# Optimization experiments

Hardware: AMD Instinct MI355X
Metric: run time of the kernel (lower is better)

## Reference

```python
import jax, jax.numpy as jnp
import numpy as np

# Module config (matches init_kwargs)
SHAPE = (32, 32)          # wire grid
KERNEL = (3, 3)           # window per dim
NUM_LAYERS = 4
NINPUTS = int(np.prod(KERNEL))        # 9
NPOS = 2 ** NINPUTS                   # 512 possible boolean input combos


def _bitmask():
    # itertools.product(range(2), repeat=NINPUTS) then transpose -> (NINPUTS, NPOS)
    # combination j, window-element m has bit (j >> (NINPUTS-1-m)) & 1
    j = jnp.arange(NPOS)
    m = jnp.arange(NINPUTS)
    return ((j[None, :] >> (NINPUTS - 1 - m)[:, None]) & 1).astype(jnp.float32)


def _convolve(x):
    # x: (B, H, W) -> (B, H, W, K) wrapped sliding windows (im2col via rolls),
    # faithful to ASIC.convolve with kernel_offset='center'.
    out = x
    for d, k in enumerate(KERNEL):
        # window element i along dim d comes from position +i (wraparound)
        out = jnp.stack([jnp.roll(out, -i, axis=1 + d) for i in range(k)], axis=out.ndim)
    out = out.reshape(x.shape + (-1,))  # (B, H, W, K) with k0 slowest-varying
    # 'center' offset: roll by prod((k-1)//2) along the LAST spatial dim (as the torch code does)
    shift = int(np.prod([(k - 1) // 2 for k in KERNEL]))
    out = jnp.roll(out, shift, axis=len(KERNEL))  # axis = last spatial axis in (B, H, W, K)
    return out


def setup_inputs() -> dict:
    key = jax.random.key(0)
    k1, k2 = jax.random.split(key)
    x = jax.random.uniform(k1, (16,) + SHAPE, dtype=jnp.float32)
    toggle_gates = jax.random.uniform(k2, (NUM_LAYERS, NPOS) + SHAPE, dtype=jnp.float32)
    return {"x": x, "toggle_gates": toggle_gates}


def reference(x, toggle_gates):
    tw = jax.nn.sigmoid(toggle_gates)       # (L, NPOS, H, W)
    bits = _bitmask()                        # (NINPUTS, NPOS)
    # embed(): shape == x spatial shape -> stride-1 slices; initial state is x, output is full state
    state = x                                # (B, H, W)
    for layer in range(NUM_LAYERS):
        conv = _convolve(state)              # (B, H, W, K)
        # soft-LUT weights: prod over window elems of (1 - |bit - input|)
        w = jnp.prod(1.0 - jnp.abs(conv[..., None] - bits), axis=-2)  # (B, H, W, NPOS)
        state = jnp.clip(jnp.einsum('bhwp,phw->bhw', w, tw[layer]), 0.0, 1.0)
    return state
```

## Files before the change

### kernel.cpp

```cpp
#include <hip/hip_runtime.h>

#define HH 32
#define WW 32
#define NB 16
#define NPOS 512
#define TILE 8
#define PPAD 516
#define NTHR 512

__global__ __launch_bounds__(NTHR) void asic_layer(
    const float* __restrict__ src,
    const float* __restrict__ tg,
    float* __restrict__ dst)
{
    __shared__ float lut[TILE * PPAD];
    __shared__ float red[NTHR];

    const int t   = threadIdx.x;
    const int hw0 = blockIdx.x * TILE;

    #pragma unroll
    for (int k = 0; k < 8; ++k) {
        int f   = t + NTHR * k;
        int p   = f >> 3;
        int pos = f & 7;
        float g = tg[p * (HH * WW) + hw0 + pos];
        lut[pos * PPAD + p] = 1.0f / (1.0f + __expf(-g));
    }

    const int c   = t & 127;
    const int q   = t >> 7;
    const int b   = c >> 3;
    const int hwl = c & 7;
    const int h   = hw0 >> 5;
    const int w   = (hw0 & 31) + hwl;

    float cc[9];
    const float* sb = src + b * (HH * WW);
    #pragma unroll
    for (int i = 0; i < 3; ++i) {
        int row = ((h + i) & 31) * 32;
        #pragma unroll
        for (int j = 0; j < 3; ++j) {
            cc[3 * i + j] = sb[row + ((w + j - 1 + 32) & 31)];
        }
    }

    __syncthreads();

    float v[32];
    {
        float a2[2], a4[4], a8[8], a16[16];
        a2[0] = 1.0f - cc[4]; a2[1] = cc[4];
        #pragma unroll
        for (int i = 0; i < 2; ++i)  { a4[2*i]  = a2[i]  * (1.0f - cc[5]); a4[2*i+1]  = a2[i]  * cc[5]; }
        #pragma unroll
        for (int i = 0; i < 4; ++i)  { a8[2*i]  = a4[i]  * (1.0f - cc[6]); a8[2*i+1]  = a4[i]  * cc[6]; }
        #pragma unroll
        for (int i = 0; i < 8; ++i)  { a16[2*i] = a8[i]  * (1.0f - cc[7]); a16[2*i+1] = a8[i]  * cc[7]; }
        #pragma unroll
        for (int i = 0; i < 16; ++i) { v[2*i]   = a16[i] * (1.0f - cc[8]); v[2*i+1]   = a16[i] * cc[8]; }
    }
    float u[16];
    {
        float a2[2], a4[4], a8[8];
        a2[0] = 1.0f - cc[0]; a2[1] = cc[0];
        #pragma unroll
        for (int i = 0; i < 2; ++i) { a4[2*i] = a2[i] * (1.0f - cc[1]); a4[2*i+1] = a2[i] * cc[1]; }
        #pragma unroll
        for (int i = 0; i < 4; ++i) { a8[2*i] = a4[i] * (1.0f - cc[2]); a8[2*i+1] = a4[i] * cc[2]; }
        #pragma unroll
        for (int i = 0; i < 8; ++i) { u[2*i]  = a8[i] * (1.0f - cc[3]); u[2*i+1]  = a8[i] * cc[3]; }
    }

    const float4* lut4 = (const float4*)(lut + hwl * PPAD);
    float acc = 0.0f;
    #pragma unroll
    for (int hh = 0; hh < 4; ++hh) {
        int hi = 4 * q + hh;
        float ps0 = 0.f, ps1 = 0.f, ps2 = 0.f, ps3 = 0.f;
        #pragma unroll
        for (int l4 = 0; l4 < 8; ++l4) {
            float4 L = lut4[hi * 8 + l4];
            ps0 = fmaf(L.x, v[4*l4+0], ps0);
            ps1 = fmaf(L.y, v[4*l4+1], ps1);
            ps2 = fmaf(L.z, v[4*l4+2], ps2);
            ps3 = fmaf(L.w, v[4*l4+3], ps3);
        }
        acc = fmaf(u[hi], (ps0 + ps1) + (ps2 + ps3), acc);
    }

    red[t] = acc;
    __syncthreads();

    if (t < 128) {
        float s = (red[t] + red[t + 128]) + (red[t + 256] + red[t + 384]);
        s = fminf(fmaxf(s, 0.0f), 1.0f);
        dst[b * (HH * WW) + h * 32 + w] = s;
    }
}

extern "C" void kernel_launch(void* const* d_in, const int* in_sizes, int n_in,
                              void* d_out, int out_size, void* d_ws, size_t ws_size,
                              hipStream_t stream) {
    const float* x  = (const float*)d_in[0];
    const float* tg = (const float*)d_in[1];
    float* out = (float*)d_out;
    float* ws  = (float*)d_ws;

    const int grid = (HH * WW) / TILE;
    const size_t L = (size_t)NPOS * HH * WW;

    asic_layer<<<grid, NTHR, 0, stream>>>(x,   tg + 0 * L, ws);
    asic_layer<<<grid, NTHR, 0, stream>>>(ws,  tg + 1 * L, out);
    asic_layer<<<grid, NTHR, 0, stream>>>(out, tg + 2 * L, ws);
    asic_layer<<<grid, NTHR, 0, stream>>>(ws,  tg + 3 * L, out);
}
```

Baseline: 78.30 us.

## Fuse four layer launches into one persistent kernel with grid barriers

Merges the four per-layer kernel launches into a single persistent kernel of 128 blocks. Each block prefetches and sigmoids the LUT slices for all four layers into shared memory up front, and a global atomic counter barrier separates the layers. This removes three launch gaps and lets the toggle-gate loads for later layers overlap with earlier work. In exchange it uses four times the LDS per block, adds a memset, and depends on all 128 blocks being co-resident for the spin barrier to be safe.

```diff
diff --git a/kernel.cpp b/kernel.cpp
--- a/kernel.cpp
+++ b/kernel.cpp
@@ -7,26 +7,33 @@
 #define TILE 8
 #define PPAD 516
 #define NTHR 512
+#define NBLK 128
+#define NLAYERS 4
 
-__global__ __launch_bounds__(NTHR) void asic_layer(
-    const float* __restrict__ src,
+__device__ __forceinline__ void grid_barrier(int* cnt) {
+    __syncthreads();
+    if (threadIdx.x == 0) {
+        __hip_atomic_fetch_add(cnt, 1, __ATOMIC_RELEASE, __HIP_MEMORY_SCOPE_AGENT);
+        while (__hip_atomic_load(cnt, __ATOMIC_ACQUIRE, __HIP_MEMORY_SCOPE_AGENT) < NBLK) {
+            __builtin_amdgcn_s_sleep(16);
+        }
+    }
+    __syncthreads();
+}
+
+__global__ __launch_bounds__(NTHR) void asic_fused(
+    const float* __restrict__ x,
     const float* __restrict__ tg,
-    float* __restrict__ dst)
+    float* __restrict__ bufA,
+    float* __restrict__ bufB,
+    float* __restrict__ out,
+    int* __restrict__ bar)
 {
-    __shared__ float lut[TILE * PPAD];
+    __shared__ float lut[NLAYERS][TILE * PPAD];
     __shared__ float red[NTHR];
 
     const int t   = threadIdx.x;
     const int hw0 = blockIdx.x * TILE;
-
-    #pragma unroll
-    for (int k = 0; k < 8; ++k) {
-        int f   = t + NTHR * k;
-        int p   = f >> 3;
-        int pos = f & 7;
-        float g = tg[p * (HH * WW) + hw0 + pos];
-        lut[pos * PPAD + p] = 1.0f / (1.0f + __expf(-g));
-    }
 
     const int c   = t & 127;
     const int q   = t >> 7;
@@ -35,68 +42,89 @@
     const int h   = hw0 >> 5;
     const int w   = (hw0 & 31) + hwl;
 
-    float cc[9];
-    const float* sb = src + b * (HH * WW);
     #pragma unroll
-    for (int i = 0; i < 3; ++i) {
-        int row = ((h + i) & 31) * 32;
-        #pragma unroll
-        for (int j = 0; j < 3; ++j) {
-            cc[3 * i + j] = sb[row + ((w + j - 1 + 32) & 31)];
-        }
+    for (int k = 0; k < 32; ++k) {
+        int f     = t + NTHR * k;
+        int layer = f >> 12;
+        int r     = f & 4095;
+        int p     = r >> 3;
+        int pos   = r & 7;
+        float g = tg[(size_t)layer * NPOS * HH * WW + p * (HH * WW) + hw0 + pos];
+        lut[layer][pos * PPAD + p] = 1.0f / (1.0f + __expf(-g));
     }
 
-    __syncthreads();
+    const float* src = x;
 
-    float v[32];
-    {
-        float a2[2], a4[4], a8[8], a16[16];
-        a2[0] = 1.0f - cc[4]; a2[1] = cc[4];
+    for (int layer = 0; layer < NLAYERS; ++layer) {
+        float* dst = (layer == 3) ? out : ((layer & 1) ? bufB : bufA);
+
+        float cc[9];
+        const float* sb = src + b * (HH * WW);
         #pragma unroll
-        for (int i = 0; i < 2; ++i)  { a4[2*i]  = a2[i]  * (1.0f - cc[5]); a4[2*i+1]  = a2[i]  * cc[5]; }
+        for (int i = 0; i < 3; ++i) {
+            int row = ((h + i) & 31) * 32;
+            #pragma unroll
+            for (int j = 0; j < 3; ++j) {
+                cc[3 * i + j] = sb[row + ((w + j - 1 + 32) & 31)];
+            }
+        }
+
+        if (layer == 0) __syncthreads();
+
+        float v[32];
+        {
+            float a2[2], a4[4], a8[8], a16[16];
+            a2[0] = 1.0f - cc[4]; a2[1] = cc[4];
+            #pragma unroll
+            for (int i = 0; i < 2; ++i)  { a4[2*i]  = a2[i]  * (1.0f - cc[5]); a4[2*i+1]  = a2[i]  * cc[5]; }
+            #pragma unroll
+            for (int i = 0; i < 4; ++i)  { a8[2*i]  = a4[i]  * (1.0f - cc[6]); a8[2*i+1]  = a4[i]  * cc[6]; }
+            #pragma unroll
+            for (int i = 0; i < 8; ++i)  { a16[2*i] = a8[i]  * (1.0f - cc[7]); a16[2*i+1] = a8[i]  * cc[7]; }
+            #pragma unroll
+            for (int i = 0; i < 16; ++i) { v[2*i]   = a16[i] * (1.0f - cc[8]); v[2*i+1]   = a16[i] * cc[8]; }
+        }
+        float u[16];
+        {
+            float a2[2], a4[4], a8[8];
+            a2[0] = 1.0f - cc[0]; a2[1] = cc[0];
+            #pragma unroll
+            for (int i = 0; i < 2; ++i) { a4[2*i] = a2[i] * (1.0f - cc[1]); a4[2*i+1] = a2[i] * cc[1]; }
+            #pragma unroll
+            for (int i = 0; i < 4; ++i) { a8[2*i] = a4[i] * (1.0f - cc[2]); a8[2*i+1] = a4[i] * cc[2]; }
+            #pragma unroll
+            for (int i = 0; i < 8; ++i) { u[2*i]  = a8[i] * (1.0f - cc[3]); u[2*i+1]  = a8[i] * cc[3]; }
+        }
+
+        const float4* lut4 = (const float4*)(&lut[layer][0] + hwl * PPAD);
+        float acc = 0.0f;
         #pragma unroll
-        for (int i = 0; i < 4; ++i)  { a8[2*i]  = a4[i]  * (1.0f - cc[6]); a8[2*i+1]  = a4[i]  * cc[6]; }
-        #pragma unroll
-        for (int i = 0; i < 8; ++i)  { a16[2*i] = a8[i]  * (1.0f - cc[7]); a16[2*i+1] = a8[i]  * cc[7]; }
-        #pragma unroll
-        for (int i = 0; i < 16; ++i) { v[2*i]   = a16[i] * (1.0f - cc[8]); v[2*i+1]   = a16[i] * cc[8]; }
-    }
-    float u[16];
-    {
-        float a2[2], a4[4], a8[8];
-        a2[0] = 1.0f - cc[0]; a2[1] = cc[0];
-        #pragma unroll
-        for (int i = 0; i < 2; ++i) { a4[2*i] = a2[i] * (1.0f - cc[1]); a4[2*i+1] = a2[i] * cc[1]; }
-        #pragma unroll
-        for (int i = 0; i < 4; ++i) { a8[2*i] = a4[i] * (1.0f - cc[2]); a8[2*i+1] = a4[i] * cc[2]; }
-        #pragma unroll
-        for (int i = 0; i < 8; ++i) { u[2*i]  = a8[i] * (1.0f - cc[3]); u[2*i+1]  = a8[i] * cc[3]; }
-    }
+        for (int hh = 0; hh < 4; ++hh) {
+            int hi = 4 * q + hh;
+            float ps0 = 0.f, ps1 = 0.f, ps2 = 0.f, ps3 = 0.f;
+            #pragma unroll
+            for (int l4 = 0; l4 < 8; ++l4) {
+                float4 L = lut4[hi * 8 + l4];
+                ps0 = fmaf(L.x, v[4*l4+0], ps0);
+                ps1 = fmaf(L.y, v[4*l4+1], ps1);
+                ps2 = fmaf(L.z, v[4*l4+2], ps2);
+                ps3 = fmaf(L.w, v[4*l4+3], ps3);
+            }
+            acc = fmaf(u[hi], (ps0 + ps1) + (ps2 + ps3), acc);
+        }
 
-    const float4* lut4 = (const float4*)(lut + hwl * PPAD);
-    float acc = 0.0f;
-    #pragma unroll
-    for (int hh = 0; hh < 4; ++hh) {
-        int hi = 4 * q + hh;
-        float ps0 = 0.f, ps1 = 0.f, ps2 = 0.f, ps3 = 0.f;
-        #pragma unroll
-        for (int l4 = 0; l4 < 8; ++l4) {
-            float4 L = lut4[hi * 8 + l4];
-            ps0 = fmaf(L.x, v[4*l4+0], ps0);
-            ps1 = fmaf(L.y, v[4*l4+1], ps1);
-            ps2 = fmaf(L.z, v[4*l4+2], ps2);
-            ps3 = fmaf(L.w, v[4*l4+3], ps3);
+        __syncthreads();
+        red[t] = acc;
+        __syncthreads();
+
+        if (t < 128) {
+            float s = (red[t] + red[t + 128]) + (red[t + 256] + red[t + 384]);
+            s = fminf(fmaxf(s, 0.0f), 1.0f);
+            dst[b * (HH * WW) + h * 32 + w] = s;
         }
-        acc = fmaf(u[hi], (ps0 + ps1) + (ps2 + ps3), acc);
-    }
 
-    red[t] = acc;
-    __syncthreads();
-
-    if (t < 128) {
-        float s = (red[t] + red[t + 128]) + (red[t + 256] + red[t + 384]);
-        s = fminf(fmaxf(s, 0.0f), 1.0f);
-        dst[b * (HH * WW) + h * 32 + w] = s;
+        if (layer < NLAYERS - 1) grid_barrier(bar + layer);
+        src = dst;
     }
 }
 
@@ -105,14 +133,11 @@
                               hipStream_t stream) {
     const float* x  = (const float*)d_in[0];
     const float* tg = (const float*)d_in[1];
-    float* out = (float*)d_out;
-    float* ws  = (float*)d_ws;
+    float* out  = (float*)d_out;
+    float* bufA = (float*)d_ws;
+    float* bufB = bufA + NB * HH * WW;
+    int*   bar  = (int*)((char*)d_ws + 256 * 1024);
 
-    const int grid = (HH * WW) / TILE;
-    const size_t L = (size_t)NPOS * HH * WW;
-
-    asic_layer<<<grid, NTHR, 0, stream>>>(x,   tg + 0 * L, ws);
-    asic_layer<<<grid, NTHR, 0, stream>>>(ws,  tg + 1 * L, out);
-    asic_layer<<<grid, NTHR, 0, stream>>>(out, tg + 2 * L, ws);
-    asic_layer<<<grid, NTHR, 0, stream>>>(ws,  tg + 3 * L, out);
+    hipMemsetAsync(bar, 0, 4 * sizeof(int), stream);
+    asic_fused<<<NBLK, NTHR, 0, stream>>>(x, tg, bufA, bufB, out, bar);
 }
```

Measured after the change: 92.11 us. 17.6% more time.

## Fuse pairs of layers into one kernel with halo recomputation in shared memory

Applied to the files above, without the earlier changes.

Each block now computes two consecutive layers. It first evaluates the earlier layer over a 3x10 halo of positions for all batches, keeps those results in shared memory, then runs the second layer on them. This halves the number of kernel launches and skips the global round trip of the intermediate state. The cost is more gate loads and sigmoids per block (38 LUT columns instead of 8), a larger shared-memory footprint that limits occupancy, and a serial full 512-term dot product per thread in the halo phase.

```diff
diff --git a/kernel.cpp b/kernel.cpp
--- a/kernel.cpp
+++ b/kernel.cpp
@@ -7,77 +7,36 @@
 #define TILE 8
 #define PPAD 516
 #define NTHR 512
+#define NPA 30
+#define NPB 8
+#define NPT (NPA + NPB)
 
-__global__ __launch_bounds__(NTHR) void asic_layer(
-    const float* __restrict__ src,
-    const float* __restrict__ tg,
-    float* __restrict__ dst)
-{
-    __shared__ float lut[TILE * PPAD];
-    __shared__ float red[NTHR];
+__device__ __forceinline__ void make_uv(const float c[9], float* u, float* v) {
+    float a2[2], a4[4], a8[8], a16[16];
+    a2[0] = 1.0f - c[4]; a2[1] = c[4];
+    #pragma unroll
+    for (int i = 0; i < 2; ++i)  { a4[2*i]  = a2[i]  * (1.0f - c[5]); a4[2*i+1]  = a2[i]  * c[5]; }
+    #pragma unroll
+    for (int i = 0; i < 4; ++i)  { a8[2*i]  = a4[i]  * (1.0f - c[6]); a8[2*i+1]  = a4[i]  * c[6]; }
+    #pragma unroll
+    for (int i = 0; i < 8; ++i)  { a16[2*i] = a8[i]  * (1.0f - c[7]); a16[2*i+1] = a8[i]  * c[7]; }
+    #pragma unroll
+    for (int i = 0; i < 16; ++i) { v[2*i]   = a16[i] * (1.0f - c[8]); v[2*i+1]   = a16[i] * c[8]; }
+    float b2[2], b4[4], b8[8];
+    b2[0] = 1.0f - c[0]; b2[1] = c[0];
+    #pragma unroll
+    for (int i = 0; i < 2; ++i) { b4[2*i] = b2[i] * (1.0f - c[1]); b4[2*i+1] = b2[i] * c[1]; }
+    #pragma unroll
+    for (int i = 0; i < 4; ++i) { b8[2*i] = b4[i] * (1.0f - c[2]); b8[2*i+1] = b4[i] * c[2]; }
+    #pragma unroll
+    for (int i = 0; i < 8; ++i) { u[2*i]  = b8[i] * (1.0f - c[3]); u[2*i+1]  = b8[i] * c[3]; }
+}
 
-    const int t   = threadIdx.x;
-    const int hw0 = blockIdx.x * TILE;
-
-    #pragma unroll
-    for (int k = 0; k < 8; ++k) {
-        int f   = t + NTHR * k;
-        int p   = f >> 3;
-        int pos = f & 7;
-        float g = tg[p * (HH * WW) + hw0 + pos];
-        lut[pos * PPAD + p] = 1.0f / (1.0f + __expf(-g));
-    }
-
-    const int c   = t & 127;
-    const int q   = t >> 7;
-    const int b   = c >> 3;
-    const int hwl = c & 7;
-    const int h   = hw0 >> 5;
-    const int w   = (hw0 & 31) + hwl;
-
-    float cc[9];
-    const float* sb = src + b * (HH * WW);
-    #pragma unroll
-    for (int i = 0; i < 3; ++i) {
-        int row = ((h + i) & 31) * 32;
-        #pragma unroll
-        for (int j = 0; j < 3; ++j) {
-            cc[3 * i + j] = sb[row + ((w + j - 1 + 32) & 31)];
-        }
-    }
-
-    __syncthreads();
-
-    float v[32];
-    {
-        float a2[2], a4[4], a8[8], a16[16];
-        a2[0] = 1.0f - cc[4]; a2[1] = cc[4];
-        #pragma unroll
-        for (int i = 0; i < 2; ++i)  { a4[2*i]  = a2[i]  * (1.0f - cc[5]); a4[2*i+1]  = a2[i]  * cc[5]; }
-        #pragma unroll
-        for (int i = 0; i < 4; ++i)  { a8[2*i]  = a4[i]  * (1.0f - cc[6]); a8[2*i+1]  = a4[i]  * cc[6]; }
-        #pragma unroll
-        for (int i = 0; i < 8; ++i)  { a16[2*i] = a8[i]  * (1.0f - cc[7]); a16[2*i+1] = a8[i]  * cc[7]; }
-        #pragma unroll
-        for (int i = 0; i < 16; ++i) { v[2*i]   = a16[i] * (1.0f - cc[8]); v[2*i+1]   = a16[i] * cc[8]; }
-    }
-    float u[16];
-    {
-        float a2[2], a4[4], a8[8];
-        a2[0] = 1.0f - cc[0]; a2[1] = cc[0];
-        #pragma unroll
-        for (int i = 0; i < 2; ++i) { a4[2*i] = a2[i] * (1.0f - cc[1]); a4[2*i+1] = a2[i] * cc[1]; }
-        #pragma unroll
-        for (int i = 0; i < 4; ++i) { a8[2*i] = a4[i] * (1.0f - cc[2]); a8[2*i+1] = a4[i] * cc[2]; }
-        #pragma unroll
-        for (int i = 0; i < 8; ++i) { u[2*i]  = a8[i] * (1.0f - cc[3]); u[2*i+1]  = a8[i] * cc[3]; }
-    }
-
-    const float4* lut4 = (const float4*)(lut + hwl * PPAD);
+__device__ __forceinline__ float lut_dot4(const float4* lut4, const float* u, const float* v,
+                                          int hi0, int nhi) {
     float acc = 0.0f;
-    #pragma unroll
-    for (int hh = 0; hh < 4; ++hh) {
-        int hi = 4 * q + hh;
+    for (int hh = 0; hh < nhi; ++hh) {
+        int hi = hi0 + hh;
         float ps0 = 0.f, ps1 = 0.f, ps2 = 0.f, ps3 = 0.f;
         #pragma unroll
         for (int l4 = 0; l4 < 8; ++l4) {
@@ -89,14 +48,100 @@
         }
         acc = fmaf(u[hi], (ps0 + ps1) + (ps2 + ps3), acc);
     }
+    return acc;
+}
 
-    red[t] = acc;
+__global__ __launch_bounds__(NTHR) void asic_pair(
+    const float* __restrict__ src,
+    const float* __restrict__ tgA,
+    const float* __restrict__ tgB,
+    float* __restrict__ dst)
+{
+    __shared__ float lutA[NPA * PPAD];
+    __shared__ float lutB[NPB * PPAD];
+    __shared__ float mid[NPA * NB];
+    __shared__ float red[NTHR];
+
+    const int t   = threadIdx.x;
+    const int hw0 = blockIdx.x * TILE;
+    const int h   = hw0 >> 5;
+    const int w0  = hw0 & 31;
+
+    #pragma unroll 4
+    for (int k = 0; k < NPT; ++k) {
+        int f   = t + NTHR * k;
+        int p   = f / NPT;
+        int pos = f - p * NPT;
+        float g;
+        float* slot;
+        if (pos < NPA) {
+            int i  = pos / 10;
+            int jj = pos - 10 * i;
+            int rm = (h + i) & 31;
+            int cm = (w0 - 1 + jj + 32) & 31;
+            g = tgA[p * (HH * WW) + rm * 32 + cm];
+            slot = &lutA[pos * PPAD + p];
+        } else {
+            int pb = pos - NPA;
+            int cm = w0 + pb;
+            g = tgB[p * (HH * WW) + h * 32 + cm];
+            slot = &lutB[pb * PPAD + p];
+        }
+        *slot = 1.0f / (1.0f + __expf(-g));
+    }
     __syncthreads();
 
-    if (t < 128) {
-        float s = (red[t] + red[t + 128]) + (red[t + 256] + red[t + 384]);
-        s = fminf(fmaxf(s, 0.0f), 1.0f);
-        dst[b * (HH * WW) + h * 32 + w] = s;
+    if (t < NPA * NB) {
+        int pos = t >> 4;
+        int b   = t & 15;
+        int i   = pos / 10;
+        int jj  = pos - 10 * i;
+        int rm  = h + i;
+        int cmb = w0 - 1 + jj;
+
+        float c[9];
+        const float* sb = src + b * (HH * WW);
+        #pragma unroll
+        for (int ii = 0; ii < 3; ++ii) {
+            int row = ((rm + ii) & 31) * 32;
+            #pragma unroll
+            for (int ji = 0; ji < 3; ++ji) {
+                c[3 * ii + ji] = sb[row + ((cmb + ji - 1 + 32) & 31)];
+            }
+        }
+        float u[16], v[32];
+        make_uv(c, u, v);
+        float acc = lut_dot4((const float4*)(lutA + pos * PPAD), u, v, 0, 16);
+        mid[pos * NB + b] = fminf(fmaxf(acc, 0.0f), 1.0f);
+    }
+    __syncthreads();
+
+    {
+        int c128 = t & 127;
+        int q    = t >> 7;
+        int posB = c128 >> 4;
+        int b    = c128 & 15;
+
+        float c[9];
+        #pragma unroll
+        for (int wi = 0; wi < 3; ++wi) {
+            #pragma unroll
+            for (int wj = 0; wj < 3; ++wj) {
+                c[3 * wi + wj] = mid[(wi * 10 + posB + wj) * NB + b];
+            }
+        }
+        float u[16], v[32];
+        make_uv(c, u, v);
+        float acc = lut_dot4((const float4*)(lutB + posB * PPAD), u, v, 4 * q, 4);
+
+        red[t] = acc;
+        __syncthreads();
+
+        if (t < 128) {
+            float s = (red[t] + red[t + 128]) + (red[t + 256] + red[t + 384]);
+            s = fminf(fmaxf(s, 0.0f), 1.0f);
+            dst[b * (HH * WW) + h * 32 + (w0 + posB)] = s;
+        }
     }
 }
 
@@ -111,8 +156,6 @@
     const int grid = (HH * WW) / TILE;
     const size_t L = (size_t)NPOS * HH * WW;
 
-    asic_layer<<<grid, NTHR, 0, stream>>>(x,   tg + 0 * L, ws);
-    asic_layer<<<grid, NTHR, 0, stream>>>(ws,  tg + 1 * L, out);
-    asic_layer<<<grid, NTHR, 0, stream>>>(out, tg + 2 * L, ws);
-    asic_layer<<<grid, NTHR, 0, stream>>>(ws,  tg + 3 * L, out);
+    asic_pair<<<grid, NTHR, 0, stream>>>(x,  tg + 0 * L, tg + 1 * L, ws);
+    asic_pair<<<grid, NTHR, 0, stream>>>(ws, tg + 2 * L, tg + 3 * L, out);
 }
```

Result: slower. 107.2 us (+36.9%).

## Split batches across two block halves and compute two batches per thread

Applied to the files above, without the earlier changes.

The grid doubles to 256 blocks by splitting the batch into two halves. Each block keeps the full 8-position sigmoid LUT for its spatial tile. Each thread now handles two batch images and two high-index rows, reusing every LUT read across both batches and cutting the per-thread u construction to a few products. The reduction switches to float2 over 8 partitions. The cost is that the sigmoid LUT is loaded and computed twice per spatial tile, and each thread uses more registers.

```diff
diff --git a/kernel.cpp b/kernel.cpp
--- a/kernel.cpp
+++ b/kernel.cpp
@@ -2,25 +2,40 @@
 
 #define HH 32
 #define WW 32
-#define NB 16
 #define NPOS 512
 #define TILE 8
 #define PPAD 516
-#define NTHR 512
+#define NTHR 256
+#define RPAD 33
+
+__device__ __forceinline__ void make_v(const float c[9], float* v) {
+    float a2[2], a4[4], a8[8], a16[16];
+    a2[0] = 1.0f - c[4]; a2[1] = c[4];
+    #pragma unroll
+    for (int i = 0; i < 2; ++i)  { a4[2*i]  = a2[i]  * (1.0f - c[5]); a4[2*i+1]  = a2[i]  * c[5]; }
+    #pragma unroll
+    for (int i = 0; i < 4; ++i)  { a8[2*i]  = a4[i]  * (1.0f - c[6]); a8[2*i+1]  = a4[i]  * c[6]; }
+    #pragma unroll
+    for (int i = 0; i < 8; ++i)  { a16[2*i] = a8[i]  * (1.0f - c[7]); a16[2*i+1] = a8[i]  * c[7]; }
+    #pragma unroll
+    for (int i = 0; i < 16; ++i) { v[2*i]   = a16[i] * (1.0f - c[8]); v[2*i+1]   = a16[i] * c[8]; }
+}
 
 __global__ __launch_bounds__(NTHR) void asic_layer(
     const float* __restrict__ src,
     const float* __restrict__ tg,
     float* __restrict__ dst)
 {
-    __shared__ float lut[TILE * PPAD];
-    __shared__ float red[NTHR];
+    __shared__ float  lut[TILE * PPAD];
+    __shared__ float2 red[8 * RPAD];
 
-    const int t   = threadIdx.x;
-    const int hw0 = blockIdx.x * TILE;
+    const int t     = threadIdx.x;
+    const int sp    = blockIdx.x & 127;
+    const int bhalf = blockIdx.x >> 7;
+    const int hw0   = sp * TILE;
 
     #pragma unroll
-    for (int k = 0; k < 8; ++k) {
+    for (int k = 0; k < 16; ++k) {
         int f   = t + NTHR * k;
         int p   = f >> 3;
         int pos = f & 7;
@@ -28,75 +43,76 @@
         lut[pos * PPAD + p] = 1.0f / (1.0f + __expf(-g));
     }
 
-    const int c   = t & 127;
-    const int q   = t >> 7;
-    const int b   = c >> 3;
-    const int hwl = c & 7;
+    const int hwl = t & 7;
+    const int bp  = (t >> 3) & 3;
+    const int oct = t >> 5;
     const int h   = hw0 >> 5;
     const int w   = (hw0 & 31) + hwl;
+    const int b0  = bhalf * 8 + 2 * bp;
 
-    float cc[9];
-    const float* sb = src + b * (HH * WW);
+    float c0[9], c1[9];
+    const float* s0 = src + b0 * (HH * WW);
+    const float* s1 = s0 + (HH * WW);
     #pragma unroll
     for (int i = 0; i < 3; ++i) {
         int row = ((h + i) & 31) * 32;
         #pragma unroll
         for (int j = 0; j < 3; ++j) {
-            cc[3 * i + j] = sb[row + ((w + j - 1 + 32) & 31)];
+            int idx = row + ((w + j - 1 + 32) & 31);
+            c0[3 * i + j] = s0[idx];
+            c1[3 * i + j] = s1[idx];
         }
     }
 
     __syncthreads();
 
-    float v[32];
-    {
-        float a2[2], a4[4], a8[8], a16[16];
-        a2[0] = 1.0f - cc[4]; a2[1] = cc[4];
-        #pragma unroll
-        for (int i = 0; i < 2; ++i)  { a4[2*i]  = a2[i]  * (1.0f - cc[5]); a4[2*i+1]  = a2[i]  * cc[5]; }
-        #pragma unroll
-        for (int i = 0; i < 4; ++i)  { a8[2*i]  = a4[i]  * (1.0f - cc[6]); a8[2*i+1]  = a4[i]  * cc[6]; }
-        #pragma unroll
-        for (int i = 0; i < 8; ++i)  { a16[2*i] = a8[i]  * (1.0f - cc[7]); a16[2*i+1] = a8[i]  * cc[7]; }
-        #pragma unroll
-        for (int i = 0; i < 16; ++i) { v[2*i]   = a16[i] * (1.0f - cc[8]); v[2*i+1]   = a16[i] * cc[8]; }
+    float v0[32], v1[32];
+    make_v(c0, v0);
+    make_v(c1, v1);
+
+    const int bit0 = (oct >> 2) & 1, bit1 = (oct >> 1) & 1, bit2 = oct & 1;
+    float base0 = (bit0 ? c0[0] : 1.0f - c0[0]) * (bit1 ? c0[1] : 1.0f - c0[1]) * (bit2 ? c0[2] : 1.0f - c0[2]);
+    float base1 = (bit0 ? c1[0] : 1.0f - c1[0]) * (bit1 ? c1[1] : 1.0f - c1[1]) * (bit2 ? c1[2] : 1.0f - c1[2]);
+    float uA0 = base0 * (1.0f - c0[3]), uB0 = base0 * c0[3];
+    float uA1 = base1 * (1.0f - c1[3]), uB1 = base1 * c1[3];
+
+    const float4* lutp = (const float4*)(lut + hwl * PPAD);
+    const float4* A = lutp + (2 * oct) * 8;
+    const float4* B = A + 8;
+
+    float sA0 = 0.f, sA1 = 0.f, sB0 = 0.f, sB1 = 0.f;
+    #pragma unroll
+    for (int l4 = 0; l4 < 8; ++l4) {
+        float4 LA = A[l4];
+        float4 LB = B[l4];
+        sA0 = fmaf(LA.x, v0[4*l4+0], sA0); sA0 = fmaf(LA.y, v0[4*l4+1], sA0);
+        sA0 = fmaf(LA.z, v0[4*l4+2], sA0); sA0 = fmaf(LA.w, v0[4*l4+3], sA0);
+        sA1 = fmaf(LA.x, v1[4*l4+0], sA1); sA1 = fmaf(LA.y, v1[4*l4+1], sA1);
+        sA1 = fmaf(LA.z, v1[4*l4+2], sA1); sA1 = fmaf(LA.w, v1[4*l4+3], sA1);
+        sB0 = fmaf(LB.x, v0[4*l4+0], sB0); sB0 = fmaf(LB.y, v0[4*l4+1], sB0);
+        sB0 = fmaf(LB.z, v0[4*l4+2], sB0); sB0 = fmaf(LB.w, v0[4*l4+3], sB0);
+        sB1 = fmaf(LB.x, v1[4*l4+0], sB1); sB1 = fmaf(LB.y, v1[4*l4+1], sB1);
+        sB1 = fmaf(LB.z, v1[4*l4+2], sB1); sB1 = fmaf(LB.w, v1[4*l4+3], sB1);
     }
-    float u[16];
-    {
-        float a2[2], a4[4], a8[8];
-        a2[0] = 1.0f - cc[0]; a2[1] = cc[0];
-        #pragma unroll
-        for (int i = 0; i < 2; ++i) { a4[2*i] = a2[i] * (1.0f - cc[1]); a4[2*i+1] = a2[i] * cc[1]; }
-        #pragma unroll
-        for (int i = 0; i < 4; ++i) { a8[2*i] = a4[i] * (1.0f - cc[2]); a8[2*i+1] = a4[i] * cc[2]; }
-        #pragma unroll
-        for (int i = 0; i < 8; ++i) { u[2*i]  = a8[i] * (1.0f - cc[3]); u[2*i+1]  = a8[i] * cc[3]; }
-    }
+    float acc0 = fmaf(uA0, sA0, uB0 * sB0);
+    float acc1 = fmaf(uA1, sA1, uB1 * sB1);
 
-    const float4* lut4 = (const float4*)(lut + hwl * PPAD);
-    float acc = 0.0f;
-    #pragma unroll
-    for (int hh = 0; hh < 4; ++hh) {
-        int hi = 4 * q + hh;
-        float ps0 = 0.f, ps1 = 0.f, ps2 = 0.f, ps3 = 0.f;
-        #pragma unroll
-        for (int l4 = 0; l4 < 8; ++l4) {
-            float4 L = lut4[hi * 8 + l4];
-            ps0 = fmaf(L.x, v[4*l4+0], ps0);
-            ps1 = fmaf(L.y, v[4*l4+1], ps1);
-            ps2 = fmaf(L.z, v[4*l4+2], ps2);
-            ps3 = fmaf(L.w, v[4*l4+3], ps3);
-        }
-        acc = fmaf(u[hi], (ps0 + ps1) + (ps2 + ps3), acc);
-    }
-
-    red[t] = acc;
+    red[oct * RPAD + bp * 8 + hwl] = make_float2(acc0, acc1);
     __syncthreads();
 
-    if (t < 128) {
-        float s = (red[t] + red[t + 128]) + (red[t + 256] + red[t + 384]);
+    if (t < 64) {
+        int hw  = t & 7;
+        int bl  = t >> 3;
+        int bpi = bl >> 1, par = bl & 1;
+        float s = 0.0f;
+        #pragma unroll
+        for (int o = 0; o < 8; ++o) {
+            float2 r = red[o * RPAD + bpi * 8 + hw];
+            s += par ? r.y : r.x;
+        }
         s = fminf(fmaxf(s, 0.0f), 1.0f);
-        dst[b * (HH * WW) + h * 32 + w] = s;
+        int b = bhalf * 8 + bl;
+        dst[b * (HH * WW) + h * 32 + (hw0 & 31) + hw] = s;
     }
 }
 
@@ -108,7 +124,7 @@
     float* out = (float*)d_out;
     float* ws  = (float*)d_ws;
 
-    const int grid = (HH * WW) / TILE;
+    const int grid = 256;
     const size_t L = (size_t)NPOS * HH * WW;
 
     asic_layer<<<grid, NTHR, 0, stream>>>(x,   tg + 0 * L, ws);
```

New measurement: 76.30 us. 2.6% less time.
